# Kernel tuning notes

Hardware: AMD Instinct MI355X
Metric: run time of the kernel (lower is better)

## Reference

```python
import jax, jax.numpy as jnp
import numpy as np

OUT_F, IN_F = 11008, 4096
GROUP = 64                      # group_size, axis=0 grouping
G = OUT_F * IN_F // GROUP       # number of groups = 704512


def setup_inputs() -> dict:
    key = jax.random.key(0)
    ks = jax.random.split(key, 7)
    x = jax.random.normal(ks[0], (512, IN_F), dtype=jnp.float32)
    # packed 4-bit weights: two nibbles per byte, packed along the group axis
    W_q = jax.random.randint(ks[1], (GROUP // 2, G), 0, 256, dtype=jnp.int32)
    # per-group dequant params (scale = 1/quant_scale in the torch code)
    scale = jax.random.uniform(ks[2], (1, G), dtype=jnp.float32) * 0.01 + 1e-4
    zero = jax.random.uniform(ks[3], (1, G), dtype=jnp.float32) * 15.0
    # low-rank correction (LoRC): W_eff = W_dq + U @ V
    U = jax.random.normal(ks[4], (OUT_F, 32), dtype=jnp.float32) * 0.02
    V = jax.random.normal(ks[5], (32, IN_F), dtype=jnp.float32) * 0.02
    bias = jax.random.normal(ks[6], (OUT_F,), dtype=jnp.float32)
    return {"x": x, "W_q": W_q, "scale": scale, "zero": zero,
            "U": U, "V": V, "bias": bias}


def _dequantize(W_q, scale, zero):
    # unpack_4bit_u8: high nibble -> first half of rows, low nibble -> second half
    hi = ((W_q >> 4) & 0xF).astype(jnp.float32)   # [32, G]
    lo = (W_q & 0xF).astype(jnp.float32)          # [32, G]
    Wg = jnp.concatenate([hi, lo], axis=0)        # [64, G] = [group_size, G]
    W = (Wg - zero) * scale                       # per-group affine dequant
    return W.reshape(OUT_F, IN_F)


def reference(x, W_q, scale, zero, U, V, bias):
    W = _dequantize(W_q, scale, zero)             # [out, in]
    W = W + U @ V                                 # low-rank correction
    # nn.Linear semantics: out = x @ W.T + bias
    return x @ W.T + bias
```

## Files before the change

kernel.cpp:

```cpp
#include <hip/hip_runtime.h>
#include <cstdint>

typedef short  s16x8 __attribute__((ext_vector_type(8)));
typedef float  f32x4 __attribute__((ext_vector_type(4)));
typedef int    i32x4 __attribute__((ext_vector_type(4)));
typedef int    i32x2 __attribute__((ext_vector_type(2)));
typedef unsigned short u16x4 __attribute__((ext_vector_type(4)));

#define OUT_F 11008
#define IN_F  4096
#define MROWS 512
#define GQ4   176128
#define HALF  5504
#define RMOD  172

__device__ __forceinline__ unsigned short f2bf(float f) {
  unsigned u = __builtin_bit_cast(unsigned, f);
  return (unsigned short)((u + 0x8000u) >> 16);
}
__device__ __forceinline__ float bfbits(unsigned bits) {
  return __builtin_bit_cast(float, bits);
}
__device__ __forceinline__ unsigned cvtpk(float a, float b) {
  unsigned r;
  asm("v_cvt_pk_bf16_f32 %0, %1, %2" : "=v"(r) : "v"(a), "v"(b));
  return r;
}

__global__ __launch_bounds__(256) void convert_k(const float* __restrict__ x,
                                                 const float* __restrict__ U,
                                                 const float* __restrict__ scale,
                                                 const float* __restrict__ zero,
                                                 unsigned short* __restrict__ xbf,
                                                 unsigned short* __restrict__ Ubf,
                                                 f32x4* __restrict__ mz) {
  int i = blockIdx.x * 256 + threadIdx.x;
  const int NX = (MROWS * IN_F) / 4;
  const int NU = (OUT_F * 32) / 4;
  const int NS = 704512 / 4;
  if (i < NX + NU) {
    const float* src; unsigned short* dst; int idx;
    if (i < NX) { src = x; dst = xbf; idx = i; }
    else        { src = U; dst = Ubf; idx = i - NX; }
    f32x4 v = *(const f32x4*)(src + (size_t)idx * 4);
    u16x4 o;
    o[0] = f2bf(v[0]); o[1] = f2bf(v[1]); o[2] = f2bf(v[2]); o[3] = f2bf(v[3]);
    *(u16x4*)(dst + (size_t)idx * 4) = o;
  } else {
    int idx = i - NX - NU;
    if (idx >= NS) return;
    f32x4 s = *(const f32x4*)(scale + (size_t)idx * 4);
    f32x4 z = *(const f32x4*)(zero  + (size_t)idx * 4);
    f32x4 m;
#pragma unroll
    for (int e = 0; e < 4; ++e) m[e] = -(z[e] + 128.f) * s[e];
    mz[idx] = m;
  }
}

__global__ __launch_bounds__(256) void pcalc_k(const float* __restrict__ x,
                                               const float* __restrict__ V,
                                               float* __restrict__ P) {
  int m  = (blockIdx.x >> 3) * 8 + (threadIdx.x >> 5);
  int j  = threadIdx.x & 31;
  int k0 = (blockIdx.x & 7) * 512;
  const float* xr = x + (size_t)m * IN_F + k0;
  const float* vr = V + (size_t)j * IN_F + k0;
  float a = 0.f;
#pragma unroll 4
  for (int k = 0; k < 512; k += 4) {
    f32x4 xv = *(const f32x4*)(xr + k);
    f32x4 vv = *(const f32x4*)(vr + k);
    a += xv[0]*vv[0] + xv[1]*vv[1] + xv[2]*vv[2] + xv[3]*vv[3];
  }
  atomicAdd(P + m * 32 + j, a);
}

__global__ __launch_bounds__(512, 6) void milo_gemm(
    const unsigned short* __restrict__ xbf,
    const i32x4*          __restrict__ Wq4,
    const f32x4*          __restrict__ Sc4,
    const f32x4*          __restrict__ Mz4,
    const float*          __restrict__ Pf,
    const i32x4*          __restrict__ Ubf4,
    const float*          __restrict__ bias,
    float*                __restrict__ out)
{
  extern __shared__ __align__(16) unsigned short smem[];

  const int tid  = threadIdx.x;
  const int lane = tid & 63;
  const int wid  = tid >> 6;
  const int wm   = wid >> 1;
  const int wn   = wid & 1;

  const int b  = blockIdx.x;
  const int L  = (b & 7) * 86 + (b >> 3);
  const int gn = L >> 2;
  const int gm = L & 3;
  const int m0 = gm * 128;
  const int o0 = gn * 32;

  const int tr = tid >> 4;
  unsigned wq_off, sc_off;
  {
    int o = o0 + tr;
    int g = o / RMOD;
    int r = o - g * RMOD;
    wq_off = (unsigned)g * GQ4 + (unsigned)r * 1024u + (tid & 15);
    sc_off = (unsigned)r * 1024u + (tid & 15);
  }
  unsigned a_src[2];
#pragma unroll
  for (int it = 0; it < 2; ++it) {
    int row   = wid * 16 + it * 8 + (lane >> 3);
    int chunk = (lane & 7) ^ (lane >> 3);
    a_src[it] = (unsigned)(m0 + row) * IN_F + chunk * 8;
  }

  const int akey   = (lane & 7) << 3;
  const int a_base = (wm * 32 + (lane & 15)) * 64 + ((lane >> 4) * 8);
  const int b_base = (wn * 32 + (lane & 15)) * 64 + ((lane >> 4) * 8);

  f32x4 acc[2][2];
  {
    f32x4 zf = {0.f, 0.f, 0.f, 0.f};
#pragma unroll
    for (int i = 0; i < 2; ++i)
#pragma unroll
      for (int j = 0; j < 2; ++j) acc[i][j] = zf;
  }

  i32x4 wq; f32x4 s4, mz4;
  f32x4 pf[2]; i32x4 uuF;

  auto issueA = [&](int buf, int k0s) {
    unsigned short* Adst = smem + buf * 8192;
#pragma unroll
    for (int it = 0; it < 2; ++it) {
      __builtin_amdgcn_global_load_lds(
          (const __attribute__((address_space(1))) unsigned int*)(xbf + a_src[it] + k0s),
          (__attribute__((address_space(3))) unsigned int*)(Adst + (wid * 16 + it * 8) * 64),
          16, 0, 0);
    }
  };
  auto loadB = [&](int kq) {
    wq  = Wq4[wq_off + kq];
    s4  = Sc4[sc_off + kq];
    mz4 = Mz4[sc_off + kq];
  };
  auto writeB = [&](int buf) {
    unsigned short* Bn = smem + 16384 + buf * 4096;
    int scol = ((tid & 15) * 4) ^ ((tr & 7) << 3);
    float h[4], l[4];
#pragma unroll
    for (int e = 0; e < 4; ++e) {
      int v = wq[e];
      float qh = bfbits(0x43000000u | (((unsigned)v & 0xF0u) << 12));
      float ql = bfbits(0x43000000u | (((unsigned)v & 0x0Fu) << 16));
      h[e] = __builtin_fmaf(qh, s4[e], mz4[e]);
      l[e] = __builtin_fmaf(ql, s4[e], mz4[e]);
    }
    i32x2 hh = { (int)cvtpk(h[0], h[1]), (int)cvtpk(h[2], h[3]) };
    i32x2 ll = { (int)cvtpk(l[0], l[1]), (int)cvtpk(l[2], l[3]) };
    *(i32x2*)(Bn + tr * 64 + scol)        = hh;
    *(i32x2*)(Bn + (tr + 32) * 64 + scol) = ll;
  };
  auto loadF = [&]() {
    int row = tid >> 2, h4 = tid & 3;
#pragma unroll
    for (int q = 0; q < 2; ++q)
      pf[q] = *(const f32x4*)(Pf + (m0 + row) * 32 + h4 * 8 + q * 4);
    int rw = tid >> 3, h8 = tid & 7;
    int oc = (rw < 32) ? (o0 + rw) : (HALF + o0 + rw - 32);
    uuF = Ubf4[oc * 4 + (h8 & 3)];
  };
  auto writeF = [&](int buf) {
    unsigned short* An = smem + buf * 8192;
    unsigned short* Bn = smem + 16384 + buf * 4096;
    i32x4 zi = {0, 0, 0, 0};
    {
      int row = tid >> 2, h4 = tid & 3;
      int key = (row & 7) << 3;
      i32x4 t4 = { (int)cvtpk(pf[0][0], pf[0][1]), (int)cvtpk(pf[0][2], pf[0][3]),
                   (int)cvtpk(pf[1][0], pf[1][1]), (int)cvtpk(pf[1][2], pf[1][3]) };
      *(i32x4*)(An + row * 64 + ((h4 * 8) ^ key))      = t4;
      *(i32x4*)(An + row * 64 + ((32 + h4 * 8) ^ key)) = zi;
    }
    {
      int rw = tid >> 3, h8 = tid & 7;
      int key = (rw & 7) << 3;
      *(i32x4*)(Bn + rw * 64 + ((h8 * 8) ^ key)) = (h8 < 4) ? uuF : zi;
    }
  };
  auto compute = [&](int buf) {
    const unsigned short* Ac = smem + buf * 8192;
    const unsigned short* Bc = smem + 16384 + buf * 4096;
    __builtin_amdgcn_s_setprio(1);
#pragma unroll
    for (int kk = 0; kk < 64; kk += 32) {
      s16x8 av[2], bv[2];
#pragma unroll
      for (int f = 0; f < 2; ++f)
        av[f] = *(const s16x8*)(Ac + ((a_base + f * 1024 + kk) ^ akey));
#pragma unroll
      for (int f = 0; f < 2; ++f)
        bv[f] = *(const s16x8*)(Bc + ((b_base + f * 1024 + kk) ^ akey));
#pragma unroll
      for (int i = 0; i < 2; ++i)
#pragma unroll
        for (int j = 0; j < 2; ++j)
          acc[i][j] = __builtin_amdgcn_mfma_f32_16x16x32_bf16(av[i], bv[j], acc[i][j], 0, 0, 0);
    }
    __builtin_amdgcn_s_setprio(0);
  };

  loadB(0);
  issueA(0, 0);
  writeB(0);
  __syncthreads();

  for (int t = 0; t < 63; ++t) {
    int cur = t & 1, nxt = cur ^ 1;
    loadB((t + 1) * 16);
    issueA(nxt, (t + 1) * 64);
    compute(cur);
    writeB(nxt);
    __syncthreads();
  }
  loadF();
  compute(1);
  writeF(0);
  __syncthreads();
  compute(0);

#pragma unroll
  for (int fn = 0; fn < 2; ++fn) {
    int c = wn * 32 + fn * 16 + (lane & 15);
    int o = (c < 32) ? (o0 + c) : (HALF + o0 + (c - 32));
    float bv = bias[o];
#pragma unroll
    for (int fm = 0; fm < 2; ++fm) {
      int m = m0 + wm * 32 + fm * 16 + ((lane >> 4) << 2);
#pragma unroll
      for (int j = 0; j < 4; ++j)
        out[(size_t)(m + j) * OUT_F + o] = acc[fm][fn][j] + bv;
    }
  }
}

extern "C" void kernel_launch(void* const* d_in, const int* in_sizes, int n_in,
                              void* d_out, int out_size, void* d_ws, size_t ws_size,
                              hipStream_t stream) {
  const float* x     = (const float*)d_in[0];
  const int*   Wq    = (const int*)d_in[1];
  const float* scale = (const float*)d_in[2];
  const float* zero  = (const float*)d_in[3];
  const float* U     = (const float*)d_in[4];
  const float* V     = (const float*)d_in[5];
  const float* bias  = (const float*)d_in[6];
  float* out = (float*)d_out;

  unsigned short* xbf = (unsigned short*)d_ws;
  unsigned short* Ubf = xbf + (size_t)MROWS * IN_F;
  float*          P   = (float*)(Ubf + (size_t)OUT_F * 32);
  float*          mz  = P + (size_t)MROWS * 32;

  (void)hipMemsetAsync(P, 0, (size_t)MROWS * 32 * sizeof(float), stream);
  convert_k<<<3080, 256, 0, stream>>>(x, U, scale, zero, xbf, Ubf, (f32x4*)mz);
  pcalc_k<<<512, 256, 0, stream>>>(x, V, P);
  milo_gemm<<<688, 512, 49152, stream>>>(xbf, (const i32x4*)Wq,
                                         (const f32x4*)scale, (const f32x4*)mz,
                                         P, (const i32x4*)Ubf, bias, out);
}
```

Before: 142.6 us.

## Pre-dequantize weights to bf16 buffer and use a streaming GEMM

Adds a separate kernel that dequantizes the 4-bit weights into a swizzled bf16 matrix in workspace. A new GEMM then loads both operands straight into LDS with async global-to-LDS loads and uses a 64x128 tile. The GEMM no longer does in-loop dequant math and register-staged B writes. The cost is an extra ~90MB bf16 write and read through HBM, and the new path runs only when the workspace is large enough, falling back to the fused kernel otherwise.

```diff
diff --git a/kernel.cpp b/kernel.cpp
--- a/kernel.cpp
+++ b/kernel.cpp
@@ -29,33 +29,32 @@
 
 __global__ __launch_bounds__(256) void convert_k(const float* __restrict__ x,
                                                  const float* __restrict__ U,
-                                                 const float* __restrict__ scale,
-                                                 const float* __restrict__ zero,
                                                  unsigned short* __restrict__ xbf,
-                                                 unsigned short* __restrict__ Ubf,
-                                                 f32x4* __restrict__ mz) {
+                                                 unsigned short* __restrict__ Ubf) {
   int i = blockIdx.x * 256 + threadIdx.x;
   const int NX = (MROWS * IN_F) / 4;
   const int NU = (OUT_F * 32) / 4;
-  const int NS = 704512 / 4;
-  if (i < NX + NU) {
-    const float* src; unsigned short* dst; int idx;
-    if (i < NX) { src = x; dst = xbf; idx = i; }
-    else        { src = U; dst = Ubf; idx = i - NX; }
-    f32x4 v = *(const f32x4*)(src + (size_t)idx * 4);
-    u16x4 o;
-    o[0] = f2bf(v[0]); o[1] = f2bf(v[1]); o[2] = f2bf(v[2]); o[3] = f2bf(v[3]);
-    *(u16x4*)(dst + (size_t)idx * 4) = o;
-  } else {
-    int idx = i - NX - NU;
-    if (idx >= NS) return;
-    f32x4 s = *(const f32x4*)(scale + (size_t)idx * 4);
-    f32x4 z = *(const f32x4*)(zero  + (size_t)idx * 4);
-    f32x4 m;
-#pragma unroll
-    for (int e = 0; e < 4; ++e) m[e] = -(z[e] + 128.f) * s[e];
-    mz[idx] = m;
-  }
+  if (i >= NX + NU) return;
+  const float* src; unsigned short* dst; int idx;
+  if (i < NX) { src = x; dst = xbf; idx = i; }
+  else        { src = U; dst = Ubf; idx = i - NX; }
+  f32x4 v = *(const f32x4*)(src + (size_t)idx * 4);
+  u16x4 o;
+  o[0] = f2bf(v[0]); o[1] = f2bf(v[1]); o[2] = f2bf(v[2]); o[3] = f2bf(v[3]);
+  *(u16x4*)(dst + (size_t)idx * 4) = o;
+}
+
+__global__ __launch_bounds__(256) void mz_k(const float* __restrict__ scale,
+                                            const float* __restrict__ zero,
+                                            f32x4* __restrict__ mz) {
+  int idx = blockIdx.x * 256 + threadIdx.x;
+  if (idx >= 176128) return;
+  f32x4 s = *(const f32x4*)(scale + (size_t)idx * 4);
+  f32x4 z = *(const f32x4*)(zero  + (size_t)idx * 4);
+  f32x4 m;
+#pragma unroll
+  for (int e = 0; e < 4; ++e) m[e] = -(z[e] + 128.f) * s[e];
+  mz[idx] = m;
 }
 
 __global__ __launch_bounds__(256) void pcalc_k(const float* __restrict__ x,
@@ -76,6 +75,195 @@
   atomicAdd(P + m * 32 + j, a);
 }
 
+__global__ __launch_bounds__(256) void wdeq_k(const i32x4* __restrict__ Wq4,
+                                              const float* __restrict__ scale,
+                                              const float* __restrict__ zero,
+                                              unsigned short* __restrict__ Wbf) {
+  int n  = blockIdx.x * 256 + threadIdx.x;
+  int jo = n / 88064;
+  int ch = n - jo * 88064;
+  int r  = ch >> 9;
+  const int chL = ch & 511;
+  const int cc0 = ch * 8;
+  f32x4 s0 = *(const f32x4*)(scale + cc0);
+  f32x4 s1 = *(const f32x4*)(scale + cc0 + 4);
+  f32x4 z0 = *(const f32x4*)(zero + cc0);
+  f32x4 z1 = *(const f32x4*)(zero + cc0 + 4);
+  float sv[8], mzv[8];
+#pragma unroll
+  for (int e = 0; e < 4; ++e) {
+    sv[e]      = s0[e]; mzv[e]     = -(z0[e] + 128.f) * s0[e];
+    sv[e + 4]  = s1[e]; mzv[e + 4] = -(z1[e] + 128.f) * s1[e];
+  }
+#pragma unroll
+  for (int jj = 0; jj < 8; ++jj) {
+    int j = jo * 8 + jj;
+    i32x4 w0 = Wq4[(size_t)j * GQ4 + ch * 2];
+    i32x4 w1 = Wq4[(size_t)j * GQ4 + ch * 2 + 1];
+    float h[8], l[8];
+#pragma unroll
+    for (int e = 0; e < 8; ++e) {
+      int v = (e < 4) ? w0[e] : w1[e - 4];
+      float qh = bfbits(0x43000000u | (((unsigned)v & 0xF0u) << 12));
+      float ql = bfbits(0x43000000u | (((unsigned)v & 0x0Fu) << 16));
+      h[e] = __builtin_fmaf(qh, sv[e], mzv[e]);
+      l[e] = __builtin_fmaf(ql, sv[e], mzv[e]);
+    }
+    i32x4 hh = { (int)cvtpk(h[0], h[1]), (int)cvtpk(h[2], h[3]),
+                 (int)cvtpk(h[4], h[5]), (int)cvtpk(h[6], h[7]) };
+    i32x4 ll = { (int)cvtpk(l[0], l[1]), (int)cvtpk(l[2], l[3]),
+                 (int)cvtpk(l[4], l[5]), (int)cvtpk(l[6], l[7]) };
+    int o  = j * RMOD + r;
+    int o2 = o + HALF;
+    unsigned sc  = ((unsigned)chL & ~7u) | (((unsigned)chL ^ (unsigned)o)  & 7u);
+    unsigned sc2 = ((unsigned)chL & ~7u) | (((unsigned)chL ^ (unsigned)o2) & 7u);
+    *(i32x4*)(Wbf + (size_t)o  * IN_F + sc  * 8) = hh;
+    *(i32x4*)(Wbf + (size_t)o2 * IN_F + sc2 * 8) = ll;
+  }
+}
+
+__global__ __launch_bounds__(512, 6) void gemm_fast(
+    const unsigned short* __restrict__ xbf,
+    const unsigned short* __restrict__ Wbf,
+    const float*          __restrict__ Pf,
+    const i32x4*          __restrict__ Ubf4,
+    const float*          __restrict__ bias,
+    float*                __restrict__ out)
+{
+  extern __shared__ __align__(16) unsigned short smem[];
+
+  const int tid  = threadIdx.x;
+  const int lane = tid & 63;
+  const int wid  = tid >> 6;
+  const int wm   = wid >> 2;
+  const int wn   = wid & 3;
+
+  const int b  = blockIdx.x;
+  const int L  = (b & 7) * 86 + (b >> 3);
+  const int gn = L >> 3;
+  const int gm = L & 7;
+  const int m0 = gm * 64;
+  const int o0 = gn * 128;
+
+  const int arow = tid >> 3;
+  const unsigned a_src = (unsigned)(m0 + arow) * IN_F +
+                         (((tid & 7) ^ (arow & 7)) * 8);
+  size_t b_src[2];
+#pragma unroll
+  for (int it = 0; it < 2; ++it)
+    b_src[it] = (size_t)(o0 + it * 64 + (tid >> 3)) * IN_F + (tid & 7) * 8;
+
+  const int akey   = (lane & 7) << 3;
+  const int a_base = (wm * 32 + (lane & 15)) * 64 + ((lane >> 4) * 8);
+  const int b_base = (wn * 32 + (lane & 15)) * 64 + ((lane >> 4) * 8);
+
+  f32x4 acc[2][2];
+  {
+    f32x4 zf = {0.f, 0.f, 0.f, 0.f};
+#pragma unroll
+    for (int i = 0; i < 2; ++i)
+#pragma unroll
+      for (int j = 0; j < 2; ++j) acc[i][j] = zf;
+  }
+  f32x4 pf0, pf1; i32x4 uuF;
+
+  auto issueA = [&](int buf, int k0s) {
+    unsigned short* Adst = smem + buf * 4096;
+    __builtin_amdgcn_global_load_lds(
+        (const __attribute__((address_space(1))) unsigned int*)(xbf + a_src + k0s),
+        (__attribute__((address_space(3))) unsigned int*)(Adst + tid * 8),
+        16, 0, 0);
+  };
+  auto issueB = [&](int buf, int k0s) {
+    unsigned short* Bdst = smem + 8192 + buf * 8192;
+#pragma unroll
+    for (int it = 0; it < 2; ++it) {
+      __builtin_amdgcn_global_load_lds(
+          (const __attribute__((address_space(1))) unsigned int*)(Wbf + b_src[it] + k0s),
+          (__attribute__((address_space(3))) unsigned int*)(Bdst + it * 4096 + tid * 8),
+          16, 0, 0);
+    }
+  };
+  auto compute = [&](int buf) {
+    const unsigned short* Ac = smem + buf * 4096;
+    const unsigned short* Bc = smem + 8192 + buf * 8192;
+    __builtin_amdgcn_s_setprio(1);
+#pragma unroll
+    for (int kk = 0; kk < 64; kk += 32) {
+      s16x8 av[2], bv[2];
+#pragma unroll
+      for (int f = 0; f < 2; ++f)
+        av[f] = *(const s16x8*)(Ac + ((a_base + f * 1024 + kk) ^ akey));
+#pragma unroll
+      for (int f = 0; f < 2; ++f)
+        bv[f] = *(const s16x8*)(Bc + ((b_base + f * 1024 + kk) ^ akey));
+#pragma unroll
+      for (int i = 0; i < 2; ++i)
+#pragma unroll
+        for (int j = 0; j < 2; ++j)
+          acc[i][j] = __builtin_amdgcn_mfma_f32_16x16x32_bf16(av[i], bv[j], acc[i][j], 0, 0, 0);
+    }
+    __builtin_amdgcn_s_setprio(0);
+  };
+  auto loadF = [&]() {
+    int row = tid >> 3, h8 = tid & 7;
+    if (h8 < 4) {
+      pf0 = *(const f32x4*)(Pf + (m0 + row) * 32 + h8 * 8);
+      pf1 = *(const f32x4*)(Pf + (m0 + row) * 32 + h8 * 8 + 4);
+    }
+    int rw = tid >> 2, h4 = tid & 3;
+    uuF = Ubf4[(size_t)(o0 + rw) * 4 + h4];
+  };
+  auto writeF = [&](int buf) {
+    unsigned short* An = smem + buf * 4096;
+    unsigned short* Bn = smem + 8192 + buf * 8192;
+    i32x4 zi = {0, 0, 0, 0};
+    {
+      int row = tid >> 3, h8 = tid & 7, key = row & 7;
+      i32x4 v = zi;
+      if (h8 < 4)
+        v = i32x4{ (int)cvtpk(pf0[0], pf0[1]), (int)cvtpk(pf0[2], pf0[3]),
+                   (int)cvtpk(pf1[0], pf1[1]), (int)cvtpk(pf1[2], pf1[3]) };
+      *(i32x4*)(An + row * 64 + ((h8 ^ key) * 8)) = v;
+    }
+    {
+      int rw = tid >> 2, h4 = tid & 3, key = rw & 7;
+      *(i32x4*)(Bn + rw * 64 + ((h4 ^ key) * 8))       = uuF;
+      *(i32x4*)(Bn + rw * 64 + (((h4 + 4) ^ key) * 8)) = zi;
+    }
+  };
+
+  issueA(0, 0);
+  issueB(0, 0);
+  __syncthreads();
+
+  for (int t = 0; t < 63; ++t) {
+    int cur = t & 1, nxt = cur ^ 1;
+    issueA(nxt, (t + 1) * 64);
+    issueB(nxt, (t + 1) * 64);
+    compute(cur);
+    __syncthreads();
+  }
+  loadF();
+  compute(1);
+  writeF(0);
+  __syncthreads();
+  compute(0);
+
+#pragma unroll
+  for (int fn = 0; fn < 2; ++fn) {
+    int o = o0 + wn * 32 + fn * 16 + (lane & 15);
+    float bv = bias[o];
+#pragma unroll
+    for (int fm = 0; fm < 2; ++fm) {
+      int m = m0 + wm * 32 + fm * 16 + ((lane >> 4) << 2);
+#pragma unroll
+      for (int j = 0; j < 4; ++j)
+        out[(size_t)(m + j) * OUT_F + o] = acc[fm][fn][j] + bv;
+    }
+  }
+}
+
 __global__ __launch_bounds__(512, 6) void milo_gemm(
     const unsigned short* __restrict__ xbf,
     const i32x4*          __restrict__ Wq4,
@@ -87,20 +275,17 @@
     float*                __restrict__ out)
 {
   extern __shared__ __align__(16) unsigned short smem[];
-
   const int tid  = threadIdx.x;
   const int lane = tid & 63;
   const int wid  = tid >> 6;
   const int wm   = wid >> 1;
   const int wn   = wid & 1;
-
   const int b  = blockIdx.x;
   const int L  = (b & 7) * 86 + (b >> 3);
   const int gn = L >> 2;
   const int gm = L & 3;
   const int m0 = gm * 128;
   const int o0 = gn * 32;
-
   const int tr = tid >> 4;
   unsigned wq_off, sc_off;
   {
@@ -117,11 +302,9 @@
     int chunk = (lane & 7) ^ (lane >> 3);
     a_src[it] = (unsigned)(m0 + row) * IN_F + chunk * 8;
   }
-
   const int akey   = (lane & 7) << 3;
   const int a_base = (wm * 32 + (lane & 15)) * 64 + ((lane >> 4) * 8);
   const int b_base = (wn * 32 + (lane & 15)) * 64 + ((lane >> 4) * 8);
-
   f32x4 acc[2][2];
   {
     f32x4 zf = {0.f, 0.f, 0.f, 0.f};
@@ -130,10 +313,8 @@
 #pragma unroll
       for (int j = 0; j < 2; ++j) acc[i][j] = zf;
   }
-
   i32x4 wq; f32x4 s4, mz4;
   f32x4 pf[2]; i32x4 uuF;
-
   auto issueA = [&](int buf, int k0s) {
     unsigned short* Adst = smem + buf * 8192;
 #pragma unroll
@@ -214,12 +395,10 @@
     }
     __builtin_amdgcn_s_setprio(0);
   };
-
   loadB(0);
   issueA(0, 0);
   writeB(0);
   __syncthreads();
-
   for (int t = 0; t < 63; ++t) {
     int cur = t & 1, nxt = cur ^ 1;
     loadB((t + 1) * 16);
@@ -233,7 +412,6 @@
   writeF(0);
   __syncthreads();
   compute(0);
-
 #pragma unroll
   for (int fn = 0; fn < 2; ++fn) {
     int c = wn * 32 + fn * 16 + (lane & 15);
@@ -264,12 +442,25 @@
   unsigned short* xbf = (unsigned short*)d_ws;
   unsigned short* Ubf = xbf + (size_t)MROWS * IN_F;
   float*          P   = (float*)(Ubf + (size_t)OUT_F * 32);
-  float*          mz  = P + (size_t)MROWS * 32;
+  char*           rest = (char*)(P + (size_t)MROWS * 32);
+  const size_t base   = (size_t)MROWS * IN_F * 2 + (size_t)OUT_F * 32 * 2
+                      + (size_t)MROWS * 32 * 4;
+  const size_t wbf_sz = (size_t)OUT_F * IN_F * 2;
 
   (void)hipMemsetAsync(P, 0, (size_t)MROWS * 32 * sizeof(float), stream);
-  convert_k<<<3080, 256, 0, stream>>>(x, U, scale, zero, xbf, Ubf, (f32x4*)mz);
+  convert_k<<<2392, 256, 0, stream>>>(x, U, xbf, Ubf);
   pcalc_k<<<512, 256, 0, stream>>>(x, V, P);
-  milo_gemm<<<688, 512, 49152, stream>>>(xbf, (const i32x4*)Wq,
-                                         (const f32x4*)scale, (const f32x4*)mz,
-                                         P, (const i32x4*)Ubf, bias, out);
-}
+
+  if (ws_size >= base + wbf_sz) {
+    unsigned short* Wbf = (unsigned short*)rest;
+    wdeq_k<<<1376, 256, 0, stream>>>((const i32x4*)Wq, scale, zero, Wbf);
+    gemm_fast<<<688, 512, 49152, stream>>>(xbf, Wbf, P, (const i32x4*)Ubf,
+                                           bias, out);
+  } else {
+    float* mz = (float*)rest;
+    mz_k<<<688, 256, 0, stream>>>(scale, zero, (f32x4*)mz);
+    milo_gemm<<<688, 512, 49152, stream>>>(xbf, (const i32x4*)Wq,
+                                           (const f32x4*)scale, (const f32x4*)mz,
+                                           P, (const i32x4*)Ubf, bias, out);
+  }
+}
```

New measurement: 137.3 us. 1.04x faster.
